# Kernel tuning notes

Measured on AMD Instinct MI355X. Metric: run time of the kernel, lower is better.

The kernel has to match this reference:

```python
import jax, jax.numpy as jnp
import numpy as np

NEG_INF = -1e30
D_MODEL = 128


def setup_inputs() -> dict:
    key = jax.random.key(0)
    k1, k2, k3 = jax.random.split(key, 3)
    B, D, Lc, Lq = 64, D_MODEL, 1024, 256
    C = jax.random.normal(k1, (B, D, Lc), dtype=jnp.float32)
    Q = jax.random.normal(k2, (B, D, Lq), dtype=jnp.float32)
    cmask = jnp.ones((B, Lc), dtype=jnp.float32)
    qmask = jnp.ones((B, Lq), dtype=jnp.float32)
    lim = (1.0 / D) ** 0.5
    w = jax.random.uniform(k3, (3 * D,), dtype=jnp.float32, minval=-lim, maxval=lim)
    return {"C": C, "Q": Q, "cmask": cmask, "qmask": qmask, "w": w}


def reference(C, Q, cmask, qmask, w):
    # C: (B, D, Lc), Q: (B, D, Lq), w: (3D,)
    D = C.shape[1]
    Ct = jnp.swapaxes(C, 1, 2)  # (B, Lc, D)
    Qt = jnp.swapaxes(Q, 1, 2)  # (B, Lq, D)
    w1, w2, w3 = w[:D], w[D:2 * D], w[2 * D:]
    # Decomposed trilinear similarity: equivalent to cat([Ct,Qt,Ct*Qt]) @ w
    S = (jnp.einsum('bld,d->bl', Ct, w1)[:, :, None]
         + jnp.einsum('bmd,d->bm', Qt, w2)[:, None, :]
         + jnp.einsum('bld,bmd->blm', Ct * w3, Qt))  # (B, Lc, Lq)
    qm = qmask[:, None, :]  # (B, 1, Lq)
    cm = cmask[:, :, None]  # (B, Lc, 1)
    S1 = jax.nn.softmax(S + (1.0 - qm) * NEG_INF, axis=2)
    S2 = jax.nn.softmax(S + (1.0 - cm) * NEG_INF, axis=1)
    A = jnp.einsum('blm,bmd->bld', S1, Qt)  # (B, Lc, D)
    S12 = jnp.einsum('blm,bnm->bln', S1, S2)  # (B, Lc, Lc)
    Bv = jnp.einsum('bln,bnd->bld', S12, Ct)  # (B, Lc, D)
    out = jnp.concatenate([Ct, A, Ct * A, Ct * Bv], axis=2)  # (B, Lc, 4D)
    # dropout is identity in eval mode
    return jnp.swapaxes(out, 1, 2)  # (B, 4D, Lc)
```

## Files before the change

kernel.cpp:

```cpp
#include <hip/hip_runtime.h>

#define NB  64
#define ND  128
#define NLC 1024
#define NLQ 256
#define FNEG (-1e30f)

typedef __bf16 bf16x8 __attribute__((ext_vector_type(8)));
typedef float f32x4 __attribute__((ext_vector_type(4)));

__device__ __forceinline__ ushort f2bf(float x) {
  unsigned u = __float_as_uint(x);
  return (ushort)((u + 0x7fffu + ((u >> 16) & 1u)) >> 16);
}
__device__ __forceinline__ float bf2f(ushort u) {
  return __uint_as_float((unsigned)u << 16);
}
__device__ __forceinline__ bf16x8 ldfrag(const ushort* p) {
  return *reinterpret_cast<const bf16x8*>(p);
}
__device__ __forceinline__ uint4 pack8(float a0, float a1, float a2, float a3,
                                       float a4, float a5, float a6, float a7) {
  uint4 pk;
  pk.x = (unsigned)f2bf(a0) | ((unsigned)f2bf(a1) << 16);
  pk.y = (unsigned)f2bf(a2) | ((unsigned)f2bf(a3) << 16);
  pk.z = (unsigned)f2bf(a4) | ((unsigned)f2bf(a5) << 16);
  pk.w = (unsigned)f2bf(a6) | ((unsigned)f2bf(a7) << 16);
  return pk;
}

__global__ __launch_bounds__(256) void convert_kernel(
    const float* __restrict__ C, const float* __restrict__ Q,
    const float* __restrict__ w,
    ushort* __restrict__ Ctw3, ushort* __restrict__ Qt16,
    ushort* __restrict__ Cn16, ushort* __restrict__ Qn16,
    float* __restrict__ c1part, float* __restrict__ q2part,
    float* __restrict__ out) {
  __shared__ float tile[64][65];
  __shared__ float cred[64][4];
  int b = blockIdx.y;
  int tid = blockIdx.x;
  int t = threadIdx.x, c = t & 63, r0 = t >> 6;
  if (tid < 32) {
    int d0 = (tid >> 4) * 64, l0 = (tid & 15) * 64;
    const float* src = C + (size_t)b * ND * NLC;
    float* o0 = out + (size_t)b * 4 * ND * NLC;
    float part = 0.f;
#pragma unroll
    for (int p = 0; p < 16; ++p) {
      int r = r0 + p * 4;
      float v = src[(size_t)(d0 + r) * NLC + l0 + c];
      tile[c][r] = v * w[2 * ND + d0 + r];
      part += v * w[d0 + r];
      o0[(size_t)(d0 + r) * NLC + l0 + c] = v;
    }
    cred[c][r0] = part;
    __syncthreads();
    ushort* dst = Ctw3 + (size_t)b * NLC * ND;
#pragma unroll
    for (int p = 0; p < 16; ++p) {
      int r = r0 + p * 4;
      dst[(size_t)(l0 + r) * ND + d0 + c] = f2bf(tile[r][c]);
    }
    if (t < 64)
      c1part[(size_t)(tid >> 4) * NB * NLC + b * NLC + l0 + t] =
          cred[t][0] + cred[t][1] + cred[t][2] + cred[t][3];
  } else if (tid < 40) {
    int q = tid - 32;
    int d0 = (q >> 2) * 64, m0 = (q & 3) * 64;
    const float* src = Q + (size_t)b * ND * NLQ;
    float part = 0.f;
#pragma unroll
    for (int p = 0; p < 16; ++p) {
      int r = r0 + p * 4;
      float v = src[(size_t)(d0 + r) * NLQ + m0 + c];
      tile[c][r] = v;
      part += v * w[ND + d0 + r];
    }
    cred[c][r0] = part;
    __syncthreads();
    ushort* dst = Qt16 + (size_t)b * NLQ * ND;
#pragma unroll
    for (int p = 0; p < 16; ++p) {
      int r = r0 + p * 4;
      dst[(size_t)(m0 + r) * ND + d0 + c] = f2bf(tile[r][c]);
    }
    if (t < 64)
      q2part[(size_t)(q >> 2) * NB * NLQ + b * NLQ + m0 + t] =
          cred[t][0] + cred[t][1] + cred[t][2] + cred[t][3];
  } else if (tid < 56) {
    size_t ofs = (size_t)(tid - 40) * 8192;
    const float* src = C + (size_t)b * ND * NLC + ofs;
    ushort* dst = Cn16 + (size_t)b * ND * NLC + ofs;
#pragma unroll
    for (int it = 0; it < 4; ++it) {
      int e = (it * 256 + t) * 8;
      float4 v0 = *(const float4*)(src + e), v1 = *(const float4*)(src + e + 4);
      *(uint4*)(dst + e) = pack8(v0.x, v0.y, v0.z, v0.w, v1.x, v1.y, v1.z, v1.w);
    }
  } else {
    size_t ofs = (size_t)(tid - 56) * 16384;
    const float* src = Q + (size_t)b * ND * NLQ + ofs;
    ushort* dst = Qn16 + (size_t)b * ND * NLQ + ofs;
#pragma unroll
    for (int it = 0; it < 8; ++it) {
      int e = (it * 256 + t) * 8;
      float4 v0 = *(const float4*)(src + e), v1 = *(const float4*)(src + e + 4);
      *(uint4*)(dst + e) = pack8(v0.x, v0.y, v0.z, v0.w, v1.x, v1.y, v1.z, v1.w);
    }
  }
}

__global__ __launch_bounds__(512, 4) void score_stats(
    const ushort* __restrict__ Ctw3, const ushort* __restrict__ Qt16,
    const ushort* __restrict__ Cn16,
    const float* __restrict__ c1part, const float* __restrict__ q2part,
    const float* __restrict__ cmask, const float* __restrict__ qmask,
    ushort* __restrict__ e1g, float* __restrict__ rscale_g,
    float* __restrict__ psum_part, float* __restrict__ chunkmax_g,
    float* __restrict__ Tpart) {
  __shared__ union {
    struct { __align__(16) ushort As[128 * 32]; __align__(16) ushort Bs[256 * 32]; } s;
    struct { float rowred[128][4]; float rowsum[128][4]; float colred[256][2]; } red;
    __align__(16) ushort bounce[128 * 264];
    __align__(16) ushort bounce2[256 * 136];
  } u;
  __shared__ float rmaxs[128];
  __shared__ float rcs[128];
  __shared__ float cnegs[128];
  __shared__ float qnegs[256];
  __shared__ float c1s[128];
  __shared__ float q2s[256];
  __shared__ float chunkmax_s;

  int b = blockIdx.y, chunk = blockIdx.x, l0 = chunk * 128;
  int t = threadIdx.x, lane = t & 63, wid = t >> 6;
  int wy = wid >> 2, wx = wid & 3, ln = lane & 15, qd = lane >> 4;

  if (t < 128) {
    int idx = b * NLC + l0 + t;
    c1s[t] = c1part[idx] + c1part[NB * NLC + idx];
    cnegs[t] = (1.f - cmask[idx]) * FNEG;
  } else if (t < 384) {
    int m = t - 128;
    int idx = b * NLQ + m;
    q2s[m] = q2part[idx] + q2part[NB * NLQ + idx];
    qnegs[m] = (1.f - qmask[idx]) * FNEG;
  }

  const ushort* Ab = Ctw3 + (size_t)b * NLC * ND;
  const ushort* Bb = Qt16 + (size_t)b * NLQ * ND;
  f32x4 acc[4][4];
#pragma unroll
  for (int i = 0; i < 4; ++i)
#pragma unroll
    for (int j = 0; j < 4; ++j) acc[i][j] = (f32x4){0.f, 0.f, 0.f, 0.f};

  for (int kk = 0; kk < ND; kk += 32) {
#pragma unroll
    for (int p = 0; p < 3; ++p) {
      int e4 = p * 512 + t;
      if (e4 < 512) {
        int r = e4 >> 2, cc = (e4 & 3) * 8;
        *(int4*)(u.s.As + r * 32 + cc) = *(const int4*)(Ab + (size_t)(l0 + r) * ND + kk + cc);
      } else {
        int e = e4 - 512;
        int r = e >> 2, cc = (e & 3) * 8;
        *(int4*)(u.s.Bs + r * 32 + cc) = *(const int4*)(Bb + (size_t)r * ND + kk + cc);
      }
    }
    __syncthreads();
    bf16x8 af[4], bfr[4];
#pragma unroll
    for (int i = 0; i < 4; ++i) {
      af[i]  = ldfrag(u.s.As + (wy * 64 + i * 16 + ln) * 32 + qd * 8);
      bfr[i] = ldfrag(u.s.Bs + (wx * 64 + i * 16 + ln) * 32 + qd * 8);
    }
#pragma unroll
    for (int i = 0; i < 4; ++i)
#pragma unroll
      for (int j = 0; j < 4; ++j)
        acc[i][j] = __builtin_amdgcn_mfma_f32_16x16x32_bf16(af[i], bfr[j], acc[i][j], 0, 0, 0);
    __syncthreads();
  }

  float qnj[4], q2j[4];
#pragma unroll
  for (int j = 0; j < 4; ++j) {
    int m = wx * 64 + j * 16 + ln;
    qnj[j] = qnegs[m];
    q2j[j] = q2s[m];
  }
#pragma unroll
  for (int i = 0; i < 4; ++i)
#pragma unroll
    for (int r = 0; r < 4; ++r) {
      int ll = wy * 64 + i * 16 + qd * 4 + r;
      float cv = c1s[ll];
#pragma unroll
      for (int j = 0; j < 4; ++j) acc[i][j][r] += cv + q2j[j];
    }

#pragma unroll
  for (int i = 0; i < 4; ++i)
#pragma unroll
    for (int r = 0; r < 4; ++r) {
      float v = -INFINITY;
#pragma unroll
      for (int j = 0; j < 4; ++j) v = fmaxf(v, acc[i][j][r] + qnj[j]);
      v = fmaxf(v, __shfl_xor(v, 1));
      v = fmaxf(v, __shfl_xor(v, 2));
      v = fmaxf(v, __shfl_xor(v, 4));
      v = fmaxf(v, __shfl_xor(v, 8));
      if (ln == 0) u.red.rowred[wy * 64 + i * 16 + qd * 4 + r][wx] = v;
    }
  __syncthreads();
  if (t < 128) {
    float v = fmaxf(fmaxf(u.red.rowred[t][0], u.red.rowred[t][1]),
                    fmaxf(u.red.rowred[t][2], u.red.rowred[t][3]));
    rmaxs[t] = v;
    rcs[t] = v + cnegs[t];
  }
  __syncthreads();
  if (t < 64) {
    float v = fmaxf(rcs[t], rcs[t + 64]);
    v = fmaxf(v, __shfl_xor(v, 1));
    v = fmaxf(v, __shfl_xor(v, 2));
    v = fmaxf(v, __shfl_xor(v, 4));
    v = fmaxf(v, __shfl_xor(v, 8));
    v = fmaxf(v, __shfl_xor(v, 16));
    v = fmaxf(v, __shfl_xor(v, 32));
    if (t == 0) chunkmax_s = v;
  }
  __syncthreads();
  if (t < 128) rcs[t] = __expf(rcs[t] - chunkmax_s);
  __syncthreads();

  float cs[4] = {0.f, 0.f, 0.f, 0.f};
#pragma unroll
  for (int i = 0; i < 4; ++i)
#pragma unroll
    for (int r = 0; r < 4; ++r) {
      int ll = wy * 64 + i * 16 + qd * 4 + r;
      float rmx = rmaxs[ll], rf = rcs[ll];
      float rs = 0.f;
#pragma unroll
      for (int j = 0; j < 4; ++j) {
        float e = __expf(acc[i][j][r] + qnj[j] - rmx);
        acc[i][j][r] = e;
        rs += e;
        cs[j] += e * rf;
      }
      rs += __shfl_xor(rs, 1);
      rs += __shfl_xor(rs, 2);
      rs += __shfl_xor(rs, 4);
      rs += __shfl_xor(rs, 8);
      if (ln == 0) u.red.rowsum[ll][wx] = rs;
    }
#pragma unroll
  for (int j = 0; j < 4; ++j) {
    float v = cs[j];
    v += __shfl_xor(v, 16);
    v += __shfl_xor(v, 32);
    if (qd == 0) u.red.colred[wx * 64 + j * 16 + ln][wy] = v;
  }
  __syncthreads();
  if (t < 128)
    rscale_g[b * NLC + l0 + t] = 1.f / (u.red.rowsum[t][0] + u.red.rowsum[t][1] +
                                        u.red.rowsum[t][2] + u.red.rowsum[t][3]);
  if (t >= 256 && t < 512) {
    int m = t - 256;
    psum_part[(b * 8 + chunk) * NLQ + m] = u.red.colred[m][0] + u.red.colred[m][1];
  }
  if (t == 0) chunkmax_g[b * 8 + chunk] = chunkmax_s;
  __syncthreads();

#pragma unroll
  for (int i = 0; i < 4; ++i)
#pragma unroll
    for (int r = 0; r < 4; ++r) {
      int ll = wy * 64 + i * 16 + qd * 4 + r;
#pragma unroll
      for (int j = 0; j < 4; ++j)
        u.bounce[ll * 264 + wx * 64 + j * 16 + ln] = f2bf(acc[i][j][r]);
    }
  __syncthreads();
  ushort* Eb = e1g + (size_t)b * NLC * NLQ;
#pragma unroll
  for (int p = 0; p < 8; ++p) {
    int idx4 = p * 512 + t;
    int r = idx4 >> 5, c = (idx4 & 31) * 8;
    *(int4*)(Eb + (size_t)(l0 + r) * NLQ + c) = *(const int4*)(u.bounce + r * 264 + c);
  }
  __syncthreads();

#pragma unroll
  for (int i = 0; i < 4; ++i)
#pragma unroll
    for (int r = 0; r < 4; ++r) {
      int ll = wy * 64 + i * 16 + qd * 4 + r;
      float rf = rcs[ll];
#pragma unroll
      for (int j = 0; j < 4; ++j)
        u.bounce2[(wx * 64 + j * 16 + ln) * 136 + ll] = f2bf(acc[i][j][r] * rf);
    }
  __syncthreads();
  const ushort* Cb = Cn16 + (size_t)b * ND * NLC;
  f32x4 acc2[4][4];
#pragma unroll
  for (int i = 0; i < 4; ++i)
#pragma unroll
    for (int j = 0; j < 4; ++j) acc2[i][j] = (f32x4){0.f, 0.f, 0.f, 0.f};
#pragma unroll
  for (int kk = 0; kk < 4; ++kk) {
    bf16x8 af2[4], bf2[4];
#pragma unroll
    for (int i = 0; i < 4; ++i)
      af2[i] = ldfrag(Cb + (size_t)(wy * 64 + i * 16 + ln) * NLC + l0 + kk * 32 + qd * 8);
#pragma unroll
    for (int j = 0; j < 4; ++j)
      bf2[j] = ldfrag(u.bounce2 + (wx * 64 + j * 16 + ln) * 136 + kk * 32 + qd * 8);
#pragma unroll
    for (int i = 0; i < 4; ++i)
#pragma unroll
      for (int j = 0; j < 4; ++j)
        acc2[i][j] = __builtin_amdgcn_mfma_f32_16x16x32_bf16(af2[i], bf2[j], acc2[i][j], 0, 0, 0);
  }
  float* Tb = Tpart + (size_t)(b * 8 + chunk) * ND * NLQ;
#pragma unroll
  for (int i = 0; i < 4; ++i)
#pragma unroll
    for (int r = 0; r < 4; ++r) {
      int d = wy * 64 + i * 16 + qd * 4 + r;
#pragma unroll
      for (int j = 0; j < 4; ++j) {
        int m = wx * 64 + j * 16 + ln;
        Tb[(size_t)d * NLQ + m] = acc2[i][j][r];
      }
    }
}

__global__ __launch_bounds__(256) void stat_combine(
    const float* __restrict__ psum_part, const float* __restrict__ chunkmax_g,
    float* __restrict__ cinv) {
  __shared__ float cm[8];
  int b = blockIdx.x, t = threadIdx.x;
  if (t < 8) cm[t] = chunkmax_g[b * 8 + t];
  __syncthreads();
  float K = cm[0];
#pragma unroll
  for (int c = 1; c < 8; ++c) K = fmaxf(K, cm[c]);
  float s = 0.f;
#pragma unroll
  for (int c = 0; c < 8; ++c)
    s += psum_part[(b * 8 + c) * NLQ + t] * __expf(cm[c] - K);
  cinv[b * NLQ + t] = 1.f / s;
}

__global__ __launch_bounds__(256) void tcombine(
    const float* __restrict__ Tpart, const float* __restrict__ cinv,
    const float* __restrict__ chunkmax_g, ushort* __restrict__ Tt) {
  int gid = blockIdx.x * 256 + threadIdx.x;
  int e = gid * 4;
  int b = e >> 15;
  int r = e & 32767;
  int m = r & 255;
  const float* cmb = chunkmax_g + b * 8;
  float K = cmb[0];
#pragma unroll
  for (int c = 1; c < 8; ++c) K = fmaxf(K, cmb[c]);
  float4 s = {0.f, 0.f, 0.f, 0.f};
#pragma unroll
  for (int c = 0; c < 8; ++c) {
    float fac = __expf(cmb[c] - K);
    float4 v = *(const float4*)(Tpart + ((size_t)(b * 8 + c)) * ND * NLQ + r);
    s.x += fac * v.x; s.y += fac * v.y; s.z += fac * v.z; s.w += fac * v.w;
  }
  float4 ci = *(const float4*)(cinv + b * NLQ + m);
  ushort4 o;
  o.x = f2bf(s.x * ci.x); o.y = f2bf(s.y * ci.y);
  o.z = f2bf(s.z * ci.z); o.w = f2bf(s.w * ci.w);
  *(ushort4*)(Tt + (size_t)b * ND * NLQ + r) = o;
}

__global__ __launch_bounds__(512, 4) void outk(
    const float* __restrict__ C, const ushort* __restrict__ Qn16,
    const ushort* __restrict__ Tt, const ushort* __restrict__ e1g,
    const float* __restrict__ rscale, float* __restrict__ out) {
  __shared__ union {
    struct { __align__(16) ushort As1[128 * 32]; __align__(16) ushort As2[128 * 32];
             __align__(16) ushort Bs[128 * 32]; } st;
    struct { float a[32][132]; float bv[32][132]; } ep;
  } u;
  int b = blockIdx.y;
  int l0 = blockIdx.x * 128;
  const ushort* Qb = Qn16 + (size_t)b * ND * NLQ;
  const ushort* Tb = Tt + (size_t)b * ND * NLQ;
  const ushort* Eb = e1g + (size_t)b * NLC * NLQ;
  int t = threadIdx.x, lane = t & 63, wid = t >> 6;
  int wy = wid >> 2, wx = wid & 3;
  int ln = lane & 15, qd = lane >> 4;
  f32x4 acc1[4][2], acc2[4][2];
#pragma unroll
  for (int i = 0; i < 4; ++i)
#pragma unroll
    for (int j = 0; j < 2; ++j) {
      acc1[i][j] = (f32x4){0.f, 0.f, 0.f, 0.f};
      acc2[i][j] = (f32x4){0.f, 0.f, 0.f, 0.f};
    }

  for (int m0 = 0; m0 < NLQ; m0 += 32) {
    {
      int r = t >> 2, cc = (t & 3) * 8;
      *(int4*)(u.st.As1 + r * 32 + cc) = *(const int4*)(Qb + (size_t)r * NLQ + m0 + cc);
      *(int4*)(u.st.As2 + r * 32 + cc) = *(const int4*)(Tb + (size_t)r * NLQ + m0 + cc);
      *(int4*)(u.st.Bs + r * 32 + cc)  = *(const int4*)(Eb + (size_t)(l0 + r) * NLQ + m0 + cc);
    }
    __syncthreads();
    bf16x8 a1[4], a2[4], bfr[2];
#pragma unroll
    for (int i = 0; i < 4; ++i) {
      a1[i] = ldfrag(u.st.As1 + (wy * 64 + i * 16 + ln) * 32 + qd * 8);
      a2[i] = ldfrag(u.st.As2 + (wy * 64 + i * 16 + ln) * 32 + qd * 8);
    }
#pragma unroll
    for (int j = 0; j < 2; ++j)
      bfr[j] = ldfrag(u.st.Bs + (wx * 32 + j * 16 + ln) * 32 + qd * 8);
#pragma unroll
    for (int i = 0; i < 4; ++i)
#pragma unroll
      for (int j = 0; j < 2; ++j) {
        acc1[i][j] = __builtin_amdgcn_mfma_f32_16x16x32_bf16(a1[i], bfr[j], acc1[i][j], 0, 0, 0);
        acc2[i][j] = __builtin_amdgcn_mfma_f32_16x16x32_bf16(a2[i], bfr[j], acc2[i][j], 0, 0, 0);
      }
    __syncthreads();
  }

  float rsj[2];
#pragma unroll
  for (int j = 0; j < 2; ++j)
    rsj[j] = rscale[b * NLC + l0 + wx * 32 + j * 16 + ln];

  const float* Cbase = C + (size_t)b * ND * NLC;
  float* outb = out + (size_t)b * 4 * ND * NLC;
#pragma unroll
  for (int db = 0; db < 4; ++db) {
    __syncthreads();
    if (wy == (db >> 1)) {
      int ibase = (db & 1) * 2;
#pragma unroll
      for (int ii = 0; ii < 2; ++ii) {
        int i = ibase + ii;
#pragma unroll
        for (int j = 0; j < 2; ++j) {
          int lc = wx * 32 + j * 16 + ln;
#pragma unroll
          for (int r = 0; r < 4; ++r) {
            int dr = ii * 16 + qd * 4 + r;
            u.ep.a[dr][lc]  = acc1[i][j][r] * rsj[j];
            u.ep.bv[dr][lc] = acc2[i][j][r] * rsj[j];
          }
        }
      }
    }
    __syncthreads();
    int row = t >> 4, colf = (t & 15) * 8;
    int d = db * 32 + row;
    const float* Crow = Cbase + (size_t)d * NLC + l0 + colf;
    float4 c0 = *(const float4*)(Crow), c1 = *(const float4*)(Crow + 4);
    float4 a0 = *(const float4*)&u.ep.a[row][colf];
    float4 a1v = *(const float4*)&u.ep.a[row][colf + 4];
    float4 b0 = *(const float4*)&u.ep.bv[row][colf];
    float4 b1 = *(const float4*)&u.ep.bv[row][colf + 4];
    float* oA = outb + (size_t)(128 + d) * NLC + l0 + colf;
    float* oCA = outb + (size_t)(256 + d) * NLC + l0 + colf;
    float* oCB = outb + (size_t)(384 + d) * NLC + l0 + colf;
    *(float4*)(oA) = a0;
    *(float4*)(oA + 4) = a1v;
    *(float4*)(oCA) = (float4){c0.x * a0.x, c0.y * a0.y, c0.z * a0.z, c0.w * a0.w};
    *(float4*)(oCA + 4) = (float4){c1.x * a1v.x, c1.y * a1v.y, c1.z * a1v.z, c1.w * a1v.w};
    *(float4*)(oCB) = (float4){c0.x * b0.x, c0.y * b0.y, c0.z * b0.z, c0.w * b0.w};
    *(float4*)(oCB + 4) = (float4){c1.x * b1.x, c1.y * b1.y, c1.z * b1.z, c1.w * b1.w};
  }
}

extern "C" void kernel_launch(void* const* d_in, const int* in_sizes, int n_in,
                              void* d_out, int out_size, void* d_ws, size_t ws_size,
                              hipStream_t stream) {
  const float* C     = (const float*)d_in[0];
  const float* Q     = (const float*)d_in[1];
  const float* cmask = (const float*)d_in[2];
  const float* qmask = (const float*)d_in[3];
  const float* w     = (const float*)d_in[4];
  float* out = (float*)d_out;

  char* p = (char*)d_ws;
  auto alloc = [&](size_t bytes) { char* r = p; p += (bytes + 255) & ~(size_t)255; return r; };
  ushort* e1g    = (ushort*)alloc((size_t)NB * NLC * NLQ * 2);
  ushort* Ctw3   = (ushort*)alloc((size_t)NB * NLC * ND * 2);
  ushort* Qt16   = (ushort*)alloc((size_t)NB * NLQ * ND * 2);
  ushort* Cn16   = (ushort*)alloc((size_t)NB * ND * NLC * 2);
  ushort* Qn16   = (ushort*)alloc((size_t)NB * ND * NLQ * 2);
  float*  Tpart  = (float*)alloc((size_t)NB * 8 * ND * NLQ * 4);
  ushort* Tt     = (ushort*)alloc((size_t)NB * ND * NLQ * 2);
  float*  c1part = (float*)alloc((size_t)2 * NB * NLC * 4);
  float*  q2part = (float*)alloc((size_t)2 * NB * NLQ * 4);
  float*  rscale = (float*)alloc((size_t)NB * NLC * 4);
  float*  cinv   = (float*)alloc((size_t)NB * NLQ * 4);
  float*  psum   = (float*)alloc((size_t)NB * 8 * NLQ * 4);
  float*  chmax  = (float*)alloc((size_t)NB * 8 * 4);

  convert_kernel<<<dim3(58, NB), 256, 0, stream>>>(C, Q, w, Ctw3, Qt16, Cn16, Qn16,
                                                   c1part, q2part, out);
  score_stats<<<dim3(NLC / 128, NB), 512, 0, stream>>>(
      Ctw3, Qt16, Cn16, c1part, q2part, cmask, qmask, e1g, rscale, psum, chmax, Tpart);
  stat_combine<<<NB, 256, 0, stream>>>(psum, chmax, cinv);
  tcombine<<<(NB * ND * NLQ / 4) / 256, 256, 0, stream>>>(Tpart, cinv, chmax, Tt);
  outk<<<dim3(NLC / 128, NB), 512, 0, stream>>>(C, Qn16, Tt, e1g, rscale, out);
}
```

Measured before the change: 267.1 us.

## Split C^T·E1 partial product into separate MFMA kernel with bf16 partials

The C·E1 product that built the T partial matrices is moved out of score_stats. score_stats now writes a transposed bf16 copy of the column-scaled exponentials, and a new tmat_mfma kernel combines two Lc chunks per block, rescaling by the chunk max, and stores bf16 partials. This cuts the fp32 Tpart traffic to a quarter (half as many partials at half the bytes) and shrinks tcombine's reads. The cost is an extra 32 MB transposed E1 write and read plus another launch, and bf16 partials lose some precision.

After: 265.4 us. Within noise of the previous version (-0.6%).

```diff
diff --git a/kernel.cpp b/kernel.cpp
--- a/kernel.cpp
+++ b/kernel.cpp
@@ -113,12 +113,11 @@
 
 __global__ __launch_bounds__(512, 4) void score_stats(
     const ushort* __restrict__ Ctw3, const ushort* __restrict__ Qt16,
-    const ushort* __restrict__ Cn16,
     const float* __restrict__ c1part, const float* __restrict__ q2part,
     const float* __restrict__ cmask, const float* __restrict__ qmask,
-    ushort* __restrict__ e1g, float* __restrict__ rscale_g,
-    float* __restrict__ psum_part, float* __restrict__ chunkmax_g,
-    float* __restrict__ Tpart) {
+    ushort* __restrict__ e1g, ushort* __restrict__ e1t,
+    float* __restrict__ rscale_g, float* __restrict__ psum_part,
+    float* __restrict__ chunkmax_g) {
   __shared__ union {
     struct { __align__(16) ushort As[128 * 32]; __align__(16) ushort Bs[256 * 32]; } s;
     struct { float rowred[128][4]; float rowsum[128][4]; float colred[256][2]; } red;
@@ -305,39 +304,14 @@
         u.bounce2[(wx * 64 + j * 16 + ln) * 136 + ll] = f2bf(acc[i][j][r] * rf);
     }
   __syncthreads();
-  const ushort* Cb = Cn16 + (size_t)b * ND * NLC;
-  f32x4 acc2[4][4];
-#pragma unroll
-  for (int i = 0; i < 4; ++i)
-#pragma unroll
-    for (int j = 0; j < 4; ++j) acc2[i][j] = (f32x4){0.f, 0.f, 0.f, 0.f};
-#pragma unroll
-  for (int kk = 0; kk < 4; ++kk) {
-    bf16x8 af2[4], bf2[4];
-#pragma unroll
-    for (int i = 0; i < 4; ++i)
-      af2[i] = ldfrag(Cb + (size_t)(wy * 64 + i * 16 + ln) * NLC + l0 + kk * 32 + qd * 8);
-#pragma unroll
-    for (int j = 0; j < 4; ++j)
-      bf2[j] = ldfrag(u.bounce2 + (wx * 64 + j * 16 + ln) * 136 + kk * 32 + qd * 8);
-#pragma unroll
-    for (int i = 0; i < 4; ++i)
-#pragma unroll
-      for (int j = 0; j < 4; ++j)
-        acc2[i][j] = __builtin_amdgcn_mfma_f32_16x16x32_bf16(af2[i], bf2[j], acc2[i][j], 0, 0, 0);
-  }
-  float* Tb = Tpart + (size_t)(b * 8 + chunk) * ND * NLQ;
-#pragma unroll
-  for (int i = 0; i < 4; ++i)
-#pragma unroll
-    for (int r = 0; r < 4; ++r) {
-      int d = wy * 64 + i * 16 + qd * 4 + r;
-#pragma unroll
-      for (int j = 0; j < 4; ++j) {
-        int m = wx * 64 + j * 16 + ln;
-        Tb[(size_t)d * NLQ + m] = acc2[i][j][r];
-      }
-    }
+  ushort* Etb = e1t + (size_t)b * NLQ * NLC;
+#pragma unroll
+  for (int p = 0; p < 8; ++p) {
+    int idx4 = p * 512 + t;
+    int m = idx4 >> 4, l8 = idx4 & 15;
+    *(int4*)(Etb + (size_t)m * NLC + l0 + l8 * 8) =
+        *(const int4*)(u.bounce2 + m * 136 + l8 * 8);
+  }
 }
 
 __global__ __launch_bounds__(256) void stat_combine(
@@ -357,11 +331,85 @@
   cinv[b * NLQ + t] = 1.f / s;
 }
 
+__global__ __launch_bounds__(512) void tmat_mfma(
+    const ushort* __restrict__ Cn16, const ushort* __restrict__ e1t,
+    const float* __restrict__ chunkmax_g, ushort* __restrict__ Tpart) {
+  __shared__ __align__(16) ushort As[128 * 32];
+  __shared__ __align__(16) ushort Bs[256 * 32];
+  int b = blockIdx.y, ks = blockIdx.x;
+  int t = threadIdx.x, lane = t & 63, wid = t >> 6;
+  int wy = wid >> 2, wx = wid & 3, ln = lane & 15, qd = lane >> 4;
+  const ushort* Cb = Cn16 + (size_t)b * ND * NLC;
+  const ushort* Eb = e1t + (size_t)b * NLQ * NLC;
+  float cm0 = chunkmax_g[b * 8 + 2 * ks];
+  float cm1 = chunkmax_g[b * 8 + 2 * ks + 1];
+  int first = (cm0 <= cm1) ? 0 : 1;
+  float resc = __expf(fminf(cm0, cm1) - fmaxf(cm0, cm1));
+  f32x4 acc[4][4];
+#pragma unroll
+  for (int i = 0; i < 4; ++i)
+#pragma unroll
+    for (int j = 0; j < 4; ++j) acc[i][j] = (f32x4){0.f, 0.f, 0.f, 0.f};
+
+  for (int h = 0; h < 2; ++h) {
+    int lbase = (2 * ks + (h ? 1 - first : first)) * 128;
+    for (int c0 = 0; c0 < 128; c0 += 32) {
+#pragma unroll
+      for (int p = 0; p < 3; ++p) {
+        int e4 = p * 512 + t;
+        if (e4 < 512) {
+          int r = e4 >> 2, cc = (e4 & 3) * 8;
+          *(int4*)(As + r * 32 + cc) =
+              *(const int4*)(Cb + (size_t)r * NLC + lbase + c0 + cc);
+        } else {
+          int e = e4 - 512;
+          int rm = e >> 2, cc = (e & 3) * 8;
+          *(int4*)(Bs + rm * 32 + cc) =
+              *(const int4*)(Eb + (size_t)rm * NLC + lbase + c0 + cc);
+        }
+      }
+      __syncthreads();
+      bf16x8 af[4], bfr[4];
+#pragma unroll
+      for (int i = 0; i < 4; ++i) {
+        af[i]  = ldfrag(As + (wy * 64 + i * 16 + ln) * 32 + qd * 8);
+        bfr[i] = ldfrag(Bs + (wx * 64 + i * 16 + ln) * 32 + qd * 8);
+      }
+#pragma unroll
+      for (int i = 0; i < 4; ++i)
+#pragma unroll
+        for (int j = 0; j < 4; ++j)
+          acc[i][j] = __builtin_amdgcn_mfma_f32_16x16x32_bf16(af[i], bfr[j], acc[i][j], 0, 0, 0);
+      __syncthreads();
+    }
+    if (h == 0) {
+#pragma unroll
+      for (int i = 0; i < 4; ++i)
+#pragma unroll
+        for (int j = 0; j < 4; ++j)
+#pragma unroll
+          for (int r = 0; r < 4; ++r) acc[i][j][r] *= resc;
+    }
+  }
+  ushort* Tb = Tpart + ((size_t)(b * 4 + ks)) * ND * NLQ;
+#pragma unroll
+  for (int i = 0; i < 4; ++i)
+#pragma unroll
+    for (int r = 0; r < 4; ++r) {
+      int d = wy * 64 + i * 16 + qd * 4 + r;
+#pragma unroll
+      for (int j = 0; j < 4; ++j) {
+        int m = wx * 64 + j * 16 + ln;
+        Tb[(size_t)d * NLQ + m] = f2bf(acc[i][j][r]);
+      }
+    }
+}
+
 __global__ __launch_bounds__(256) void tcombine(
-    const float* __restrict__ Tpart, const float* __restrict__ cinv,
+    const ushort* __restrict__ Tpart, const float* __restrict__ cinv,
     const float* __restrict__ chunkmax_g, ushort* __restrict__ Tt) {
   int gid = blockIdx.x * 256 + threadIdx.x;
-  int e = gid * 4;
+  int e = gid * 8;
   int b = e >> 15;
   int r = e & 32767;
   int m = r & 255;
@@ -369,18 +417,20 @@
   float K = cmb[0];
 #pragma unroll
   for (int c = 1; c < 8; ++c) K = fmaxf(K, cmb[c]);
-  float4 s = {0.f, 0.f, 0.f, 0.f};
-#pragma unroll
-  for (int c = 0; c < 8; ++c) {
-    float fac = __expf(cmb[c] - K);
-    float4 v = *(const float4*)(Tpart + ((size_t)(b * 8 + c)) * ND * NLQ + r);
-    s.x += fac * v.x; s.y += fac * v.y; s.z += fac * v.z; s.w += fac * v.w;
-  }
-  float4 ci = *(const float4*)(cinv + b * NLQ + m);
-  ushort4 o;
-  o.x = f2bf(s.x * ci.x); o.y = f2bf(s.y * ci.y);
-  o.z = f2bf(s.z * ci.z); o.w = f2bf(s.w * ci.w);
-  *(ushort4*)(Tt + (size_t)b * ND * NLQ + r) = o;
+  float s[8] = {0.f, 0.f, 0.f, 0.f, 0.f, 0.f, 0.f, 0.f};
+#pragma unroll
+  for (int ks = 0; ks < 4; ++ks) {
+    float fac = __expf(fmaxf(cmb[2 * ks], cmb[2 * ks + 1]) - K);
+    int4 v = *(const int4*)(Tpart + ((size_t)(b * 4 + ks)) * ND * NLQ + r);
+    const ushort* sv = (const ushort*)&v;
+#pragma unroll
+    for (int k = 0; k < 8; ++k) s[k] += fac * bf2f(sv[k]);
+  }
+  float4 ci0 = *(const float4*)(cinv + b * NLQ + m);
+  float4 ci1 = *(const float4*)(cinv + b * NLQ + m + 4);
+  *(uint4*)(Tt + (size_t)b * ND * NLQ + r) =
+      pack8(s[0] * ci0.x, s[1] * ci0.y, s[2] * ci0.z, s[3] * ci0.w,
+            s[4] * ci1.x, s[5] * ci1.y, s[6] * ci1.z, s[7] * ci1.w);
 }
 
 __global__ __launch_bounds__(512, 4) void outk(
@@ -497,11 +547,12 @@
   char* p = (char*)d_ws;
   auto alloc = [&](size_t bytes) { char* r = p; p += (bytes + 255) & ~(size_t)255; return r; };
   ushort* e1g    = (ushort*)alloc((size_t)NB * NLC * NLQ * 2);
+  ushort* e1t    = (ushort*)alloc((size_t)NB * NLQ * NLC * 2);
   ushort* Ctw3   = (ushort*)alloc((size_t)NB * NLC * ND * 2);
   ushort* Qt16   = (ushort*)alloc((size_t)NB * NLQ * ND * 2);
   ushort* Cn16   = (ushort*)alloc((size_t)NB * ND * NLC * 2);
   ushort* Qn16   = (ushort*)alloc((size_t)NB * ND * NLQ * 2);
-  float*  Tpart  = (float*)alloc((size_t)NB * 8 * ND * NLQ * 4);
+  ushort* Tpart  = (ushort*)alloc((size_t)NB * 4 * ND * NLQ * 2);
   ushort* Tt     = (ushort*)alloc((size_t)NB * ND * NLQ * 2);
   float*  c1part = (float*)alloc((size_t)2 * NB * NLC * 4);
   float*  q2part = (float*)alloc((size_t)2 * NB * NLQ * 4);
@@ -513,8 +564,9 @@
   convert_kernel<<<dim3(58, NB), 256, 0, stream>>>(C, Q, w, Ctw3, Qt16, Cn16, Qn16,
                                                    c1part, q2part, out);
   score_stats<<<dim3(NLC / 128, NB), 512, 0, stream>>>(
-      Ctw3, Qt16, Cn16, c1part, q2part, cmask, qmask, e1g, rscale, psum, chmax, Tpart);
+      Ctw3, Qt16, c1part, q2part, cmask, qmask, e1g, e1t, rscale, psum, chmax);
   stat_combine<<<NB, 256, 0, stream>>>(psum, chmax, cinv);
-  tcombine<<<(NB * ND * NLQ / 4) / 256, 256, 0, stream>>>(Tpart, cinv, chmax, Tt);
+  tmat_mfma<<<dim3(4, NB), 512, 0, stream>>>(Cn16, e1t, chmax, Tpart);
+  tcombine<<<(NB * ND * NLQ / 8) / 256, 256, 0, stream>>>(Tpart, cinv, chmax, Tt);
   outk<<<dim3(NLC / 128, NB), 512, 0, stream>>>(C, Qn16, Tt, e1g, rscale, out);
 }
```
